# Kernel optimization log

Hardware: AMD Instinct MI355X
Metric: run time of the kernel (lower is better)

The kernel has to match this reference:

```python
import jax, jax.numpy as jnp
import numpy as np

D_MODEL = 1024
N_HEADS = 16
HEAD = D_MODEL // N_HEADS
B, S = 2, 2048


def setup_inputs() -> dict:
    key = jax.random.key(0)
    ks = jax.random.split(key, 9)
    sc = 1.0 / np.sqrt(D_MODEL)
    return {
        "q": jax.random.normal(ks[0], (B, S, D_MODEL), dtype=jnp.float32),
        "k": jax.random.normal(ks[1], (B, S, D_MODEL), dtype=jnp.float32),
        "v": jax.random.normal(ks[2], (B, S, D_MODEL), dtype=jnp.float32),
        "mask": jnp.zeros((S, S), dtype=jnp.float32),
        "Wq": jax.random.normal(ks[3], (D_MODEL, D_MODEL), dtype=jnp.float32) * sc,
        "bq": jnp.zeros((D_MODEL,), dtype=jnp.float32),
        "Wk": jax.random.normal(ks[4], (D_MODEL, D_MODEL), dtype=jnp.float32) * sc,
        "bk": jnp.zeros((D_MODEL,), dtype=jnp.float32),
        "Wv": jax.random.normal(ks[5], (D_MODEL, D_MODEL), dtype=jnp.float32) * sc,
        "bv": jnpp_zeros() if False else jnp.zeros((D_MODEL,), dtype=jnp.float32),
    }


def reference(q, k, v, mask, Wq, bq, Wk, bk, Wv, bv):
    # Linear projections (torch Linear: x @ W.T + b)
    qp = q @ Wq.T + bq  # (B, S, D)
    kp = k @ Wk.T + bk
    vp = v @ Wv.T + bv
    # split heads -> (B, H, S, Hd)
    def split(x):
        return x.reshape(B, S, N_HEADS, HEAD).transpose(0, 2, 1, 3)
    qh, kh, vh = split(qp), split(kp), split(vp)
    scores = jnp.einsum('bhqd,bhkd->bhqk', qh, kh) / np.sqrt(HEAD)
    scores = scores + mask  # additive mask broadcast over (B, H)
    attn = jax.nn.softmax(scores, axis=-1)
    out = jnp.einsum('bhqk,bhkd->bhqd', attn, vh)
    return out.transpose(0, 2, 1, 3).reshape(B, S, D_MODEL)
```

## Files before the change

kernel.cpp:

```cpp
#include <hip/hip_runtime.h>
#include <cstdint>

#define DM 1024
#define NH 16
#define HDIM 64
#define SEQ 2048
#define NB 2
#define L2E 1.44269504f

typedef unsigned short u16;
typedef unsigned int u32;
typedef __attribute__((ext_vector_type(8))) short bf16x8;
typedef __attribute__((ext_vector_type(8))) unsigned short u16x8;
typedef __attribute__((ext_vector_type(4))) unsigned int u32x4;
typedef __attribute__((ext_vector_type(4))) float f32x4;
typedef __attribute__((ext_vector_type(16))) float f32x16;
typedef __attribute__((ext_vector_type(4))) unsigned short u16x4;

__device__ __forceinline__ u16 f2bf(float f) {
  uint32_t x = __float_as_uint(f);
  x += 0x7fffu + ((x >> 16) & 1u);
  return (u16)(x >> 16);
}

__device__ __forceinline__ u32 pack_bf2t(float lo, float hi) {
  return __builtin_amdgcn_perm(__float_as_uint(hi), __float_as_uint(lo), 0x07060302u);
}

__device__ __forceinline__ void gload_lds16(const void* g, void* lds) {
  __builtin_amdgcn_global_load_lds(
      (const __attribute__((address_space(1))) unsigned int*)(uintptr_t)g,
      (__attribute__((address_space(3))) unsigned int*)(uint32_t)(uintptr_t)lds,
      16, 0, 0);
}


__global__ __launch_bounds__(256) void cvt_kernel(
    const float4* __restrict__ s0, const float4* __restrict__ s1, const float4* __restrict__ s2,
    const float4* __restrict__ s3, const float4* __restrict__ s4, const float4* __restrict__ s5,
    u16x4* __restrict__ d0, u16x4* __restrict__ d1, u16x4* __restrict__ d2,
    u16x4* __restrict__ d3, u16x4* __restrict__ d4, u16x4* __restrict__ d5) {
  int i = blockIdx.x * 256 + threadIdx.x;
  const float4* s;
  u16x4* d;
  int off;
  if (i < 3 * 1048576) {
    int seg = i >> 20;
    off = i & 1048575;
    s = seg == 0 ? s0 : (seg == 1 ? s1 : s2);
    d = seg == 0 ? d0 : (seg == 1 ? d1 : d2);
  } else {
    int j = i - 3 * 1048576;
    int seg = j >> 18;
    off = j & 262143;
    s = seg == 0 ? s3 : (seg == 1 ? s4 : s5);
    d = seg == 0 ? d3 : (seg == 1 ? d4 : d5);
  }
  float4 v = s[off];
  u16x4 o = {f2bf(v.x), f2bf(v.y), f2bf(v.z), f2bf(v.w)};
  d[off] = o;
}

__global__ __launch_bounds__(256) void maskprep_kernel(const float* __restrict__ mask,
                                                       u16* __restrict__ maskP) {
  __shared__ float tile[32][257];
  const int t = threadIdx.x;
  const int q0 = blockIdx.x * 32;
#pragma unroll
  for (int ss = 0; ss < 2; ++ss) {
    const int st = blockIdx.y * 2 + ss;
    const int kv0 = st * 256;
    if (ss) __syncthreads();
#pragma unroll
    for (int p = 0; p < 8; ++p) {
      const int row = p * 4 + (t >> 6);
      const int col = (t & 63) * 4;
      *(float4*)&tile[row][col] = *(const float4*)&mask[(size_t)(q0 + row) * SEQ + kv0 + col];
    }
    __syncthreads();
    const int tgl = t >> 5, ql = t & 31;
    u16 outv[32];
#pragma unroll
    for (int i = 0; i < 32; ++i) {
      const int hl = i >> 4, r = i & 15;
      const int kvl = (r & 3) + 8 * (r >> 2) + 4 * hl;
      outv[i] = f2bf(tile[ql][tgl * 32 + kvl] * L2E);
    }
    u16* dst = maskP + ((size_t)(st * 8 + tgl) * SEQ + (q0 + ql)) * 32;
#pragma unroll
    for (int j = 0; j < 4; ++j) *(u16x8*)(dst + 8 * j) = *(const u16x8*)&outv[8 * j];
  }
}

__global__ __launch_bounds__(256) void proj_kernel(
    const u16* __restrict__ Xq, const u16* __restrict__ Xk, const u16* __restrict__ Xv,
    const u16* __restrict__ Wqp, const u16* __restrict__ Wkp, const u16* __restrict__ Wvp,
    const float* __restrict__ bqp, const float* __restrict__ bkp, const float* __restrict__ bvp,
    u16* __restrict__ Qp, u16* __restrict__ Kp, u16* __restrict__ Vt) {
  __shared__ __align__(16) u16 sA[2][128 * 32];
  __shared__ __align__(16) u16 sB[2][128 * 32];
  const int t = threadIdx.x;
  const int w = t >> 6, lane = t & 63, quad = lane >> 4, l16 = lane & 15;
  const int wr = w >> 1, wc = w & 1;
  const int m0 = blockIdx.y * 128, n0 = blockIdx.x * 128;
  const int mode = blockIdx.z;
  const u16* X = mode == 0 ? Xq : (mode == 1 ? Xk : Xv);
  const u16* W = mode == 0 ? Wqp : (mode == 1 ? Wkp : Wvp);
  const float* bias = mode == 0 ? bqp : (mode == 1 ? bkp : bvp);

  f32x4 acc[4][4] = {};
  const int srow = lane >> 2;
  const int scol = (lane & 3) * 16;

#pragma unroll
  for (int j = 0; j < 2; ++j) {
    const int rbase = (w * 2 + j) * 16;
    gload_lds16((const char*)X + ((size_t)(m0 + rbase + srow) * DM) * 2 + scol,
                (char*)sA[0] + rbase * 64);
    gload_lds16((const char*)W + ((size_t)(n0 + rbase + srow) * DM) * 2 + scol,
                (char*)sB[0] + rbase * 64);
  }

  for (int it = 0; it < 32; ++it) {
    const int p = it & 1;
    __syncthreads();
    if (it < 31) {
      const int k0 = (it + 1) * 32;
#pragma unroll
      for (int j = 0; j < 2; ++j) {
        const int rbase = (w * 2 + j) * 16;
        gload_lds16((const char*)X + ((size_t)(m0 + rbase + srow) * DM + k0) * 2 + scol,
                    (char*)sA[p ^ 1] + rbase * 64);
        gload_lds16((const char*)W + ((size_t)(n0 + rbase + srow) * DM + k0) * 2 + scol,
                    (char*)sB[p ^ 1] + rbase * 64);
      }
    }
    bf16x8 af[4], bfr[4];
#pragma unroll
    for (int i = 0; i < 4; ++i)
      af[i] = *(const bf16x8*)&sA[p][(wr * 64 + i * 16 + l16) * 32 + quad * 8];
#pragma unroll
    for (int j = 0; j < 4; ++j)
      bfr[j] = *(const bf16x8*)&sB[p][(wc * 64 + j * 16 + l16) * 32 + quad * 8];
#pragma unroll
    for (int i = 0; i < 4; ++i)
#pragma unroll
      for (int j = 0; j < 4; ++j)
        acc[i][j] = __builtin_amdgcn_mfma_f32_16x16x32_bf16(af[i], bfr[j], acc[i][j], 0, 0, 0);
  }

  float bb[4];
#pragma unroll
  for (int j = 0; j < 4; ++j) bb[j] = bias[n0 + wc * 64 + j * 16 + l16];
  const float scl = (mode == 0) ? 0.18033688011f : 1.0f;

#pragma unroll
  for (int i = 0; i < 4; ++i) {
    const int mbase = m0 + wr * 64 + i * 16 + quad * 4;
    const int bidx = mbase >> 11;
    const int s = mbase & 2047;
#pragma unroll
    for (int j = 0; j < 4; ++j) {
      const int n = n0 + wc * 64 + j * 16 + l16;
      const int h = n >> 6, hd = n & 63;
      const size_t hb = (size_t)(bidx * NH + h) * (SEQ * HDIM);
      if (mode == 2) {
        const int tv = (s >> 5) * 2048 + (hd >> 5) * 1024 + ((s >> 4) & 1) * 512 +
                       ((s >> 3) & 1) * 256 + (hd & 31) * 8 + (s & 7);
        u16x4 pk = {f2bf(acc[i][j][0] + bb[j]), f2bf(acc[i][j][1] + bb[j]),
                    f2bf(acc[i][j][2] + bb[j]), f2bf(acc[i][j][3] + bb[j])};
        *(u16x4*)&Vt[hb + tv] = pk;
      } else {
        u16* dst = (mode == 0) ? Qp : Kp;
        const int th = (s >> 5) * 2048 + (hd >> 4) * 512 + ((hd >> 3) & 1) * 256 +
                       (s & 31) * 8 + (hd & 7);
#pragma unroll
        for (int r = 0; r < 4; ++r)
          dst[hb + th + r * 8] = f2bf((acc[i][j][r] + bb[j]) * scl);
      }
    }
  }
}

__global__ __launch_bounds__(256, 2) void attn_kernel(
    const u16* __restrict__ Qp, const u16* __restrict__ Kp,
    const u16* __restrict__ Vt, const u16* __restrict__ maskP,
    float* __restrict__ out) {
  __shared__ float sO[4][32][65];
  __shared__ float sL[4][64];
  const int t = threadIdx.x, w = t >> 6, lane = t & 63;
  const int l31 = lane & 31, hl = lane >> 5;
  const int h = blockIdx.x, qt = blockIdx.y, b = blockIdx.z;
  const int q0 = qt * 64;
  const u16* Qh = Qp + (size_t)(b * NH + h) * (SEQ * HDIM);
  const u16* Kh = Kp + (size_t)(b * NH + h) * (SEQ * HDIM);
  const u16* Vh = Vt + (size_t)(b * NH + h) * (SEQ * HDIM);

  bf16x8 qf[2][4];
#pragma unroll
  for (int sub = 0; sub < 2; ++sub)
#pragma unroll
    for (int kt = 0; kt < 4; ++kt)
      qf[sub][kt] =
          *(const bf16x8*)(Qh + (size_t)((q0 >> 5) + sub) * 2048 + kt * 512 + lane * 8);

  const int Tb = w * 16;
  const u16* Kt = Kh + (size_t)Tb * 2048 + (size_t)lane * 8;
  const u16* Vw = Vh + (size_t)Tb * 2048 + (size_t)lane * 8;
  const u16* mb0 = maskP + ((size_t)Tb * SEQ + (q0 + l31)) * 32 + hl * 16;
  const u16* mb1 = mb0 + 32 * 32;

  f32x16 oacc[2][2] = {};
  float l_run[2] = {0.f, 0.f};

  bf16x8 kf[4], vf[2][2];
#pragma unroll
  for (int kt = 0; kt < 4; ++kt) kf[kt] = *(const bf16x8*)(Kt + kt * 512);
#pragma unroll
  for (int half = 0; half < 2; ++half)
#pragma unroll
    for (int ks = 0; ks < 2; ++ks)
      vf[half][ks] = *(const bf16x8*)(Vw + half * 1024 + ks * 512);
  u32x4 mk[2][2];
  mk[0][0] = *(const u32x4*)(mb0);
  mk[0][1] = *(const u32x4*)(mb0 + 8);
  mk[1][0] = *(const u32x4*)(mb1);
  mk[1][1] = *(const u32x4*)(mb1 + 8);

#pragma unroll 2
  for (int it = 0; it < 16; ++it) {
    const int itn = it < 15 ? it + 1 : 15;
    bf16x8 kfn[4], vfn[2][2];
#pragma unroll
    for (int kt = 0; kt < 4; ++kt)
      kfn[kt] = *(const bf16x8*)(Kt + (size_t)itn * 2048 + kt * 512);
#pragma unroll
    for (int half = 0; half < 2; ++half)
#pragma unroll
      for (int ks = 0; ks < 2; ++ks)
        vfn[half][ks] =
            *(const bf16x8*)(Vw + (size_t)itn * 2048 + half * 1024 + ks * 512);
    u32x4 mkn[2][2];
    mkn[0][0] = *(const u32x4*)(mb0 + (size_t)itn * (SEQ * 32));
    mkn[0][1] = *(const u32x4*)(mb0 + (size_t)itn * (SEQ * 32) + 8);
    mkn[1][0] = *(const u32x4*)(mb1 + (size_t)itn * (SEQ * 32));
    mkn[1][1] = *(const u32x4*)(mb1 + (size_t)itn * (SEQ * 32) + 8);

    bf16x8 pfr[2][2];
#pragma unroll
    for (int sub = 0; sub < 2; ++sub) {
      f32x16 st;
#pragma unroll
      for (int r = 0; r < 8; ++r) {
        const u32 word = (r < 4 ? mk[sub][0][r & 3] : mk[sub][1][r & 3]);
        st[2 * r] = __uint_as_float(word << 16);
        st[2 * r + 1] = __uint_as_float(word & 0xffff0000u);
      }
#pragma unroll
      for (int kt = 0; kt < 4; ++kt)
        st = __builtin_amdgcn_mfma_f32_32x32x16_bf16(kf[kt], qf[sub][kt], st, 0, 0, 0);

      float ls = 0.f;
#pragma unroll
      for (int r = 0; r < 16; ++r) {
        st[r] = __builtin_amdgcn_exp2f(st[r]);
        ls += st[r];
      }
      l_run[sub] += ls;

      u32 pk[4][2];
#pragma unroll
      for (int g = 0; g < 4; ++g) {
        pk[g][0] = pack_bf2t(st[4 * g + 0], st[4 * g + 1]);
        pk[g][1] = pack_bf2t(st[4 * g + 2], st[4 * g + 3]);
      }
#pragma unroll
      for (int ks = 0; ks < 2; ++ks) {
        u32 sa = hl ? pk[2 * ks][0] : pk[2 * ks + 1][0];
        u32 sb = hl ? pk[2 * ks][1] : pk[2 * ks + 1][1];
        u32 ra = __shfl_xor(sa, 32);
        u32 rb = __shfl_xor(sb, 32);
        u32 oa = hl ? pk[2 * ks + 1][0] : pk[2 * ks][0];
        u32 ob = hl ? pk[2 * ks + 1][1] : pk[2 * ks][1];
        union {
          u32 u[4];
          bf16x8 v;
        } f;
        f.u[0] = hl ? ra : oa;
        f.u[1] = hl ? rb : ob;
        f.u[2] = hl ? oa : ra;
        f.u[3] = hl ? ob : rb;
        pfr[sub][ks] = f.v;
      }
    }

#pragma unroll
    for (int sub = 0; sub < 2; ++sub)
#pragma unroll
      for (int ks = 0; ks < 2; ++ks) {
        oacc[0][sub] = __builtin_amdgcn_mfma_f32_32x32x16_bf16(vf[0][ks], pfr[sub][ks],
                                                               oacc[0][sub], 0, 0, 0);
        oacc[1][sub] = __builtin_amdgcn_mfma_f32_32x32x16_bf16(vf[1][ks], pfr[sub][ks],
                                                               oacc[1][sub], 0, 0, 0);
      }

#pragma unroll
    for (int kt = 0; kt < 4; ++kt) kf[kt] = kfn[kt];
#pragma unroll
    for (int half = 0; half < 2; ++half)
#pragma unroll
      for (int ks = 0; ks < 2; ++ks) vf[half][ks] = vfn[half][ks];
#pragma unroll
    for (int sub = 0; sub < 2; ++sub) {
      mk[sub][0] = mkn[sub][0];
      mk[sub][1] = mkn[sub][1];
    }
  }

  l_run[0] += __shfl_xor(l_run[0], 32);
  l_run[1] += __shfl_xor(l_run[1], 32);
  if (hl == 0) {
    sL[w][l31] = l_run[0];
    sL[w][32 + l31] = l_run[1];
  }

  const int hd = t & 31, grp = t >> 5;
#pragma unroll
  for (int half = 0; half < 2; ++half) {
    __syncthreads();
#pragma unroll
    for (int sub = 0; sub < 2; ++sub)
#pragma unroll
      for (int r = 0; r < 16; ++r)
        sO[w][(r & 3) + 8 * (r >> 2) + 4 * hl][sub * 32 + l31] = oacc[half][sub][r];
    __syncthreads();
#pragma unroll
    for (int p8 = 0; p8 < 8; ++p8) {
      const int qi = grp * 8 + p8;
      const float lsum = sL[0][qi] + sL[1][qi] + sL[2][qi] + sL[3][qi];
      const float val = sO[0][hd][qi] + sO[1][hd][qi] + sO[2][hd][qi] + sO[3][hd][qi];
      out[(size_t)(b * SEQ + q0 + qi) * DM + h * HDIM + half * 32 + hd] = val / lsum;
    }
  }
}

extern "C" void kernel_launch(void* const* d_in, const int* in_sizes, int n_in,
                              void* d_out, int out_size, void* d_ws, size_t ws_size,
                              hipStream_t stream) {
  const float* q = (const float*)d_in[0];
  const float* k = (const float*)d_in[1];
  const float* v = (const float*)d_in[2];
  const float* mask = (const float*)d_in[3];
  const float* Wq = (const float*)d_in[4];
  const float* bq = (const float*)d_in[5];
  const float* Wk = (const float*)d_in[6];
  const float* bk = (const float*)d_in[7];
  const float* Wv = (const float*)d_in[8];
  const float* bv = (const float*)d_in[9];

  char* ws = (char*)d_ws;
  u16* q_bf = (u16*)(ws + 0);
  u16* k_bf = (u16*)(ws + 8388608);
  u16* v_bf = (u16*)(ws + 16777216);
  u16* wq_bf = (u16*)(ws + 25165824);
  u16* wk_bf = (u16*)(ws + 27262976);
  u16* wv_bf = (u16*)(ws + 29360128);
  u16* Qp = (u16*)(ws + 31457280);
  u16* Kp = (u16*)(ws + 39845888);
  u16* Vt = (u16*)(ws + 48234496);
  u16* maskP = (u16*)(ws + 56623104);

  cvt_kernel<<<15360, 256, 0, stream>>>(
      (const float4*)q, (const float4*)k, (const float4*)v, (const float4*)Wq,
      (const float4*)Wk, (const float4*)Wv, (u16x4*)q_bf, (u16x4*)k_bf, (u16x4*)v_bf,
      (u16x4*)wq_bf, (u16x4*)wk_bf, (u16x4*)wv_bf);

  maskprep_kernel<<<dim3(64, 4), 256, 0, stream>>>(mask, maskP);

  proj_kernel<<<dim3(8, 32, 3), 256, 0, stream>>>(q_bf, k_bf, v_bf, wq_bf, wk_bf, wv_bf,
                                                  bq, bk, bv, Qp, Kp, Vt);

  attn_kernel<<<dim3(16, 32, 2), 256, 0, stream>>>(Qp, Kp, Vt, maskP, (float*)d_out);
}
```

Measured before the change: 223.0 us.

## Fuse activation bf16 conversion into projection and halve attention waves

Drops the separate conversion pass over q/k/v. The projection kernel now loads fp32 activations into registers and converts them to bf16 while writing LDS, so those tensors no longer make a round trip through global memory. The weight conversion and mask prep are merged into one launch. Separately, the attention kernel goes from 4 to 2 waves per block, each covering twice the KV range, and no longer prefetches V a tile ahead, which lowers parallelism and may expose load latency.

```diff
diff --git a/kernel.cpp b/kernel.cpp
--- a/kernel.cpp
+++ b/kernel.cpp
@@ -35,40 +35,29 @@
 }
 
 
-__global__ __launch_bounds__(256) void cvt_kernel(
-    const float4* __restrict__ s0, const float4* __restrict__ s1, const float4* __restrict__ s2,
-    const float4* __restrict__ s3, const float4* __restrict__ s4, const float4* __restrict__ s5,
+__global__ __launch_bounds__(256) void prep_kernel(
+    const float4* __restrict__ W0, const float4* __restrict__ W1, const float4* __restrict__ W2,
     u16x4* __restrict__ d0, u16x4* __restrict__ d1, u16x4* __restrict__ d2,
-    u16x4* __restrict__ d3, u16x4* __restrict__ d4, u16x4* __restrict__ d5) {
-  int i = blockIdx.x * 256 + threadIdx.x;
-  const float4* s;
-  u16x4* d;
-  int off;
-  if (i < 3 * 1048576) {
-    int seg = i >> 20;
-    off = i & 1048575;
-    s = seg == 0 ? s0 : (seg == 1 ? s1 : s2);
-    d = seg == 0 ? d0 : (seg == 1 ? d1 : d2);
-  } else {
-    int j = i - 3 * 1048576;
-    int seg = j >> 18;
-    off = j & 262143;
-    s = seg == 0 ? s3 : (seg == 1 ? s4 : s5);
-    d = seg == 0 ? d3 : (seg == 1 ? d4 : d5);
-  }
-  float4 v = s[off];
-  u16x4 o = {f2bf(v.x), f2bf(v.y), f2bf(v.z), f2bf(v.w)};
-  d[off] = o;
-}
-
-__global__ __launch_bounds__(256) void maskprep_kernel(const float* __restrict__ mask,
-                                                       u16* __restrict__ maskP) {
+    const float* __restrict__ mask, u16* __restrict__ maskP) {
+  const int bx = blockIdx.x;
+  const int t = threadIdx.x;
+  if (bx < 3072) {
+    const int i = bx * 256 + t;
+    const int seg = i >> 18, off = i & 262143;
+    const float4* s = seg == 0 ? W0 : (seg == 1 ? W1 : W2);
+    u16x4* d = seg == 0 ? d0 : (seg == 1 ? d1 : d2);
+    float4 v = s[off];
+    u16x4 o = {f2bf(v.x), f2bf(v.y), f2bf(v.z), f2bf(v.w)};
+    d[off] = o;
+    return;
+  }
   __shared__ float tile[32][257];
-  const int t = threadIdx.x;
-  const int q0 = blockIdx.x * 32;
+  const int mb = bx - 3072;
+  const int q0 = (mb & 63) * 32;
+  const int yt = mb >> 6;
 #pragma unroll
   for (int ss = 0; ss < 2; ++ss) {
-    const int st = blockIdx.y * 2 + ss;
+    const int st = yt * 2 + ss;
     const int kv0 = st * 256;
     if (ss) __syncthreads();
 #pragma unroll
@@ -93,7 +82,7 @@
 }
 
 __global__ __launch_bounds__(256) void proj_kernel(
-    const u16* __restrict__ Xq, const u16* __restrict__ Xk, const u16* __restrict__ Xv,
+    const float* __restrict__ Xq, const float* __restrict__ Xk, const float* __restrict__ Xv,
     const u16* __restrict__ Wqp, const u16* __restrict__ Wkp, const u16* __restrict__ Wvp,
     const float* __restrict__ bqp, const float* __restrict__ bkp, const float* __restrict__ bvp,
     u16* __restrict__ Qp, u16* __restrict__ Kp, u16* __restrict__ Vt) {
@@ -104,33 +93,46 @@
   const int wr = w >> 1, wc = w & 1;
   const int m0 = blockIdx.y * 128, n0 = blockIdx.x * 128;
   const int mode = blockIdx.z;
-  const u16* X = mode == 0 ? Xq : (mode == 1 ? Xk : Xv);
+  const float* X = mode == 0 ? Xq : (mode == 1 ? Xk : Xv);
   const u16* W = mode == 0 ? Wqp : (mode == 1 ? Wkp : Wvp);
   const float* bias = mode == 0 ? bqp : (mode == 1 ? bkp : bvp);
 
   f32x4 acc[4][4] = {};
+  const int ar = t >> 3;
+  const int ac = t & 7;
   const int srow = lane >> 2;
   const int scol = (lane & 3) * 16;
 
-#pragma unroll
-  for (int j = 0; j < 2; ++j) {
-    const int rbase = (w * 2 + j) * 16;
-    gload_lds16((const char*)X + ((size_t)(m0 + rbase + srow) * DM) * 2 + scol,
-                (char*)sA[0] + rbase * 64);
-    gload_lds16((const char*)W + ((size_t)(n0 + rbase + srow) * DM) * 2 + scol,
-                (char*)sB[0] + rbase * 64);
+  {
+    float4 x0[4];
+#pragma unroll
+    for (int rr = 0; rr < 4; ++rr)
+      x0[rr] = *(const float4*)&X[(size_t)(m0 + rr * 32 + ar) * DM + ac * 4];
+#pragma unroll
+    for (int rr = 0; rr < 4; ++rr) {
+      u16x4 pk = {f2bf(x0[rr].x), f2bf(x0[rr].y), f2bf(x0[rr].z), f2bf(x0[rr].w)};
+      *(u16x4*)&sA[0][(rr * 32 + ar) * 32 + ac * 4] = pk;
+    }
+#pragma unroll
+    for (int j = 0; j < 2; ++j) {
+      const int rbase = (w * 2 + j) * 16;
+      gload_lds16((const char*)W + ((size_t)(n0 + rbase + srow) * DM) * 2 + scol,
+                  (char*)sB[0] + rbase * 64);
+    }
   }
 
   for (int it = 0; it < 32; ++it) {
     const int p = it & 1;
     __syncthreads();
+    float4 xn[4];
     if (it < 31) {
       const int k0 = (it + 1) * 32;
 #pragma unroll
+      for (int rr = 0; rr < 4; ++rr)
+        xn[rr] = *(const float4*)&X[(size_t)(m0 + rr * 32 + ar) * DM + k0 + ac * 4];
+#pragma unroll
       for (int j = 0; j < 2; ++j) {
         const int rbase = (w * 2 + j) * 16;
-        gload_lds16((const char*)X + ((size_t)(m0 + rbase + srow) * DM + k0) * 2 + scol,
-                    (char*)sA[p ^ 1] + rbase * 64);
         gload_lds16((const char*)W + ((size_t)(n0 + rbase + srow) * DM + k0) * 2 + scol,
                     (char*)sB[p ^ 1] + rbase * 64);
       }
@@ -147,6 +149,13 @@
 #pragma unroll
       for (int j = 0; j < 4; ++j)
         acc[i][j] = __builtin_amdgcn_mfma_f32_16x16x32_bf16(af[i], bfr[j], acc[i][j], 0, 0, 0);
+    if (it < 31) {
+#pragma unroll
+      for (int rr = 0; rr < 4; ++rr) {
+        u16x4 pk = {f2bf(xn[rr].x), f2bf(xn[rr].y), f2bf(xn[rr].z), f2bf(xn[rr].w)};
+        *(u16x4*)&sA[p ^ 1][(rr * 32 + ar) * 32 + ac * 4] = pk;
+      }
+    }
   }
 
   float bb[4];
@@ -182,12 +191,12 @@
   }
 }
 
-__global__ __launch_bounds__(256, 2) void attn_kernel(
+__global__ __launch_bounds__(128, 2) void attn_kernel(
     const u16* __restrict__ Qp, const u16* __restrict__ Kp,
     const u16* __restrict__ Vt, const u16* __restrict__ maskP,
     float* __restrict__ out) {
-  __shared__ float sO[4][32][65];
-  __shared__ float sL[4][64];
+  __shared__ float sO[2][32][65];
+  __shared__ float sL[2][64];
   const int t = threadIdx.x, w = t >> 6, lane = t & 63;
   const int l31 = lane & 31, hl = lane >> 5;
   const int h = blockIdx.x, qt = blockIdx.y, b = blockIdx.z;
@@ -204,7 +213,7 @@
       qf[sub][kt] =
           *(const bf16x8*)(Qh + (size_t)((q0 >> 5) + sub) * 2048 + kt * 512 + lane * 8);
 
-  const int Tb = w * 16;
+  const int Tb = w * 32;
   const u16* Kt = Kh + (size_t)Tb * 2048 + (size_t)lane * 8;
   const u16* Vw = Vh + (size_t)Tb * 2048 + (size_t)lane * 8;
   const u16* mb0 = maskP + ((size_t)Tb * SEQ + (q0 + l31)) * 32 + hl * 16;
@@ -213,14 +222,9 @@
   f32x16 oacc[2][2] = {};
   float l_run[2] = {0.f, 0.f};
 
-  bf16x8 kf[4], vf[2][2];
+  bf16x8 kf[4];
 #pragma unroll
   for (int kt = 0; kt < 4; ++kt) kf[kt] = *(const bf16x8*)(Kt + kt * 512);
-#pragma unroll
-  for (int half = 0; half < 2; ++half)
-#pragma unroll
-    for (int ks = 0; ks < 2; ++ks)
-      vf[half][ks] = *(const bf16x8*)(Vw + half * 1024 + ks * 512);
   u32x4 mk[2][2];
   mk[0][0] = *(const u32x4*)(mb0);
   mk[0][1] = *(const u32x4*)(mb0 + 8);
@@ -228,18 +232,20 @@
   mk[1][1] = *(const u32x4*)(mb1 + 8);
 
 #pragma unroll 2
-  for (int it = 0; it < 16; ++it) {
-    const int itn = it < 15 ? it + 1 : 15;
-    bf16x8 kfn[4], vfn[2][2];
+  for (int it = 0; it < 32; ++it) {
+    bf16x8 vf[2][2];
+#pragma unroll
+    for (int half = 0; half < 2; ++half)
+#pragma unroll
+      for (int ks = 0; ks < 2; ++ks)
+        vf[half][ks] =
+            *(const bf16x8*)(Vw + (size_t)it * 2048 + half * 1024 + ks * 512);
+
+    const int itn = it < 31 ? it + 1 : 31;
+    bf16x8 kfn[4];
 #pragma unroll
     for (int kt = 0; kt < 4; ++kt)
       kfn[kt] = *(const bf16x8*)(Kt + (size_t)itn * 2048 + kt * 512);
-#pragma unroll
-    for (int half = 0; half < 2; ++half)
-#pragma unroll
-      for (int ks = 0; ks < 2; ++ks)
-        vfn[half][ks] =
-            *(const bf16x8*)(Vw + (size_t)itn * 2048 + half * 1024 + ks * 512);
     u32x4 mkn[2][2];
     mkn[0][0] = *(const u32x4*)(mb0 + (size_t)itn * (SEQ * 32));
     mkn[0][1] = *(const u32x4*)(mb0 + (size_t)itn * (SEQ * 32) + 8);
@@ -307,10 +313,6 @@
 #pragma unroll
     for (int kt = 0; kt < 4; ++kt) kf[kt] = kfn[kt];
 #pragma unroll
-    for (int half = 0; half < 2; ++half)
-#pragma unroll
-      for (int ks = 0; ks < 2; ++ks) vf[half][ks] = vfn[half][ks];
-#pragma unroll
     for (int sub = 0; sub < 2; ++sub) {
       mk[sub][0] = mkn[sub][0];
       mk[sub][1] = mkn[sub][1];
@@ -335,10 +337,10 @@
         sO[w][(r & 3) + 8 * (r >> 2) + 4 * hl][sub * 32 + l31] = oacc[half][sub][r];
     __syncthreads();
 #pragma unroll
-    for (int p8 = 0; p8 < 8; ++p8) {
-      const int qi = grp * 8 + p8;
-      const float lsum = sL[0][qi] + sL[1][qi] + sL[2][qi] + sL[3][qi];
-      const float val = sO[0][hd][qi] + sO[1][hd][qi] + sO[2][hd][qi] + sO[3][hd][qi];
+    for (int p16 = 0; p16 < 16; ++p16) {
+      const int qi = grp * 16 + p16;
+      const float lsum = sL[0][qi] + sL[1][qi];
+      const float val = sO[0][hd][qi] + sO[1][hd][qi];
       out[(size_t)(b * SEQ + q0 + qi) * DM + h * HDIM + half * 32 + hd] = val / lsum;
     }
   }
@@ -359,26 +361,20 @@
   const float* bv = (const float*)d_in[9];
 
   char* ws = (char*)d_ws;
-  u16* q_bf = (u16*)(ws + 0);
-  u16* k_bf = (u16*)(ws + 8388608);
-  u16* v_bf = (u16*)(ws + 16777216);
-  u16* wq_bf = (u16*)(ws + 25165824);
-  u16* wk_bf = (u16*)(ws + 27262976);
-  u16* wv_bf = (u16*)(ws + 29360128);
-  u16* Qp = (u16*)(ws + 31457280);
-  u16* Kp = (u16*)(ws + 39845888);
-  u16* Vt = (u16*)(ws + 48234496);
-  u16* maskP = (u16*)(ws + 56623104);
-
-  cvt_kernel<<<15360, 256, 0, stream>>>(
-      (const float4*)q, (const float4*)k, (const float4*)v, (const float4*)Wq,
-      (const float4*)Wk, (const float4*)Wv, (u16x4*)q_bf, (u16x4*)k_bf, (u16x4*)v_bf,
-      (u16x4*)wq_bf, (u16x4*)wk_bf, (u16x4*)wv_bf);
-
-  maskprep_kernel<<<dim3(64, 4), 256, 0, stream>>>(mask, maskP);
-
-  proj_kernel<<<dim3(8, 32, 3), 256, 0, stream>>>(q_bf, k_bf, v_bf, wq_bf, wk_bf, wv_bf,
+  u16* wq_bf = (u16*)(ws + 0);
+  u16* wk_bf = (u16*)(ws + 2097152);
+  u16* wv_bf = (u16*)(ws + 4194304);
+  u16* Qp = (u16*)(ws + 6291456);
+  u16* Kp = (u16*)(ws + 14680064);
+  u16* Vt = (u16*)(ws + 23068672);
+  u16* maskP = (u16*)(ws + 31457280);
+
+  prep_kernel<<<3328, 256, 0, stream>>>((const float4*)Wq, (const float4*)Wk,
+                                        (const float4*)Wv, (u16x4*)wq_bf, (u16x4*)wk_bf,
+                                        (u16x4*)wv_bf, mask, maskP);
+
+  proj_kernel<<<dim3(8, 32, 3), 256, 0, stream>>>(q, k, v, wq_bf, wk_bf, wv_bf,
                                                   bq, bk, bv, Qp, Kp, Vt);
 
-  attn_kernel<<<dim3(16, 32, 2), 256, 0, stream>>>(Qp, Kp, Vt, maskP, (float*)d_out);
-}
+  attn_kernel<<<dim3(16, 32, 2), 128, 0, stream>>>(Qp, Kp, Vt, maskP, (float*)d_out);
+}
```

Measured after the change: 227.6 us. 1.02x slower.
